# Kernel optimization log

Hardware: AMD Instinct MI355X
Metric: run time of the kernel (lower is better)

The kernel has to match this reference:

```python
import jax, jax.numpy as jnp
import numpy as np

B, N, K = 4, 4096, 16
DP, DM = 128, 512


def _gather(points, idx):
    # points [B,N,C], idx [B,N,K] -> [B,N,K,C] (index_points)
    b, n, k = idx.shape
    flat = jnp.take_along_axis(points, idx.reshape(b, -1)[:, :, None], axis=1)
    return flat.reshape(b, n, k, points.shape[-1])


def _mlp2(x, w1, b1, w2, b2):
    return jax.nn.relu(x @ w1 + b1) @ w2 + b2


def setup_inputs():
    key = jax.random.key(0)
    ks = jax.random.split(key, 20)
    s_dp = 1.0 / np.sqrt(DP)
    s_dm = 1.0 / np.sqrt(DM)
    return {
        "xyz": jax.random.normal(ks[0], (B, N, 3), jnp.float32),
        "features": jax.random.normal(ks[1], (B, N, DP), jnp.float32),
        "fc1_w": jax.random.normal(ks[2], (DP, DM), jnp.float32) * s_dp,
        "fc1_b": jnp.zeros((DM,), jnp.float32),
        "fc2_w": jax.random.normal(ks[3], (DM, DP), jnp.float32) * s_dm,
        "fc2_b": jnp.zeros((DP,), jnp.float32),
        "wq": jax.random.normal(ks[4], (DM, DM), jnp.float32) * s_dm,
        "wk": jax.random.normal(ks[5], (DM, DM), jnp.float32) * s_dm,
        "wv": jax.random.normal(ks[6], (DM, DM), jnp.float32) * s_dm,
        "d1_w": jax.random.normal(ks[7], (3, DM), jnp.float32) * (1.0 / np.sqrt(3.0)),
        "d1_b": jnp.zeros((DM,), jnp.float32),
        "d2_w": jax.random.normal(ks[8], (DM, DM), jnp.float32) * s_dm,
        "d2_b": jnp.zeros((DM,), jnp.float32),
        "g1_w": jax.random.normal(ks[9], (DM, DM), jnp.float32) * s_dm,
        "g1_b": jnp.zeros((DM,), jnp.float32),
        "g2_w": jax.random.normal(ks[10], (DM, DM), jnp.float32) * s_dm,
        "g2_b": jnp.zeros((DM,), jnp.float32),
    }


def reference(xyz, features, fc1_w, fc1_b, fc2_w, fc2_b, wq, wk, wv,
              d1_w, d1_b, d2_w, d2_b, g1_w, g1_b, g2_w, g2_b):
    # square_distance via ||a-b||^2 = |a|^2 + |b|^2 - 2 a.b  (avoids [B,N,N,3])
    sq = jnp.sum(xyz * xyz, axis=-1)                       # [B,N]
    dists = sq[:, :, None] + sq[:, None, :] - 2.0 * jnp.einsum('bnc,bmc->bnm', xyz, xyz)
    knn_idx = jax.lax.top_k(-dists, K)[1]                  # [B,N,K] k-nearest
    knn_xyz = _gather(xyz, knn_idx)                        # [B,N,K,3]

    pre = features
    x = features @ fc1_w + fc1_b                           # [B,N,DM]
    q = x @ wq                                             # [B,N,DM]
    k = _gather(x @ wk, knn_idx)                           # [B,N,K,DM]
    v = _gather(x @ wv, knn_idx)                           # [B,N,K,DM]

    pos_enc = _mlp2(xyz[:, :, None] - knn_xyz, d1_w, d1_b, d2_w, d2_b)  # [B,N,K,DM]
    attn = _mlp2(q[:, :, None] - k + pos_enc, g1_w, g1_b, g2_w, g2_b)   # [B,N,K,DM]
    attn = jax.nn.softmax(attn / np.sqrt(DM), axis=-2)     # softmax over neighbors
    res = jnp.sum(attn * (v + pos_enc), axis=2)            # einsum bmnf,bmnf->bmf
    res = res @ fc2_w + fc2_b + pre                        # [B,N,DP]
    return res, attn
```

## Files before the change

kernel.cpp:

```cpp
#include <hip/hip_runtime.h>

#define NPTS   4096
#define NBATCH 4
#define KNN    16
#define DMODEL 512
#define DPOINT 128
#define QKVLD  1536

#define BN 128
#define BK 64

typedef unsigned short bfu;
typedef __attribute__((ext_vector_type(8))) short short8;
typedef __attribute__((ext_vector_type(4))) float f32x4;

__device__ __forceinline__ bfu f2bf(float f) {
    unsigned u = __builtin_bit_cast(unsigned, f);
    return (bfu)((u + 0x7fffu + ((u >> 16) & 1u)) >> 16);
}
__device__ __forceinline__ float bf2f(bfu h) {
    unsigned u = ((unsigned)h) << 16;
    return __builtin_bit_cast(float, u);
}

__device__ __forceinline__ void gload_lds16(const bfu* g, bfu* l) {
    __builtin_amdgcn_global_load_lds(
        (const __attribute__((address_space(1))) void*)g,
        (__attribute__((address_space(3))) void*)l, 16, 0, 0);
}

#define TPQ 8
#define QPB 32

__device__ __forceinline__ void knn_merge_level(float* bd, int* bi, int lvl)
{
    float pd[KNN]; int pi[KNN];
#pragma unroll
    for (int i = 0; i < KNN; ++i) {
        pd[i] = __shfl_xor(bd[KNN-1-i], lvl);
        pi[i] = __shfl_xor(bi[KNN-1-i], lvl);
    }
#pragma unroll
    for (int i = 0; i < KNN; ++i) {
        bool take = (pd[i] < bd[i]) || (pd[i] == bd[i] && pi[i] < bi[i]);
        if (take) { bd[i] = pd[i]; bi[i] = pi[i]; }
    }
#pragma unroll
    for (int s = 8; s >= 1; s >>= 1) {
#pragma unroll
        for (int i = 0; i < KNN; ++i) {
            if ((i & s) == 0) {
                const int j = i + s;
                bool sw = (bd[j] < bd[i]) || (bd[j] == bd[i] && bi[j] < bi[i]);
                if (sw) {
                    float td = bd[i]; bd[i] = bd[j]; bd[j] = td;
                    int   ti = bi[i]; bi[i] = bi[j]; bi[j] = ti;
                }
            }
        }
    }
}

__global__ __launch_bounds__(256) void knn_kernel(const float* __restrict__ xyz,
                                                  int* __restrict__ knn_out)
{
    __shared__ float4 pts[NPTS];
    const int b    = blockIdx.y;
    const int tid  = threadIdx.x;
    const int qloc = tid >> 3;
    const int sub  = tid & 7;
    const int n    = blockIdx.x * QPB + qloc;

    const float* bx = xyz + (size_t)b * NPTS * 3;
    for (int i = tid; i < NPTS; i += 256) {
        float x = bx[i*3+0], y = bx[i*3+1], z = bx[i*3+2];
        pts[i] = make_float4(x, y, z, x*x + y*y + z*z);
    }
    __syncthreads();

    const float4 me = pts[n];
    float bd[KNN];
    int   bi[KNN];
#pragma unroll
    for (int i = 0; i < KNN; ++i) { bd[i] = 3.4e38f; bi[i] = -1; }

    for (int t0 = 0; t0 < NPTS / TPQ; t0 += 8) {
        float d[8];
#pragma unroll
        for (int j = 0; j < 8; ++j) {
            float4 o = pts[sub + ((t0 + j) << 3)];
            d[j] = me.w + o.w - 2.f*(me.x*o.x + me.y*o.y + me.z*o.z);
        }
        float mn = fminf(fminf(fminf(d[0],d[1]),fminf(d[2],d[3])),
                         fminf(fminf(d[4],d[5]),fminf(d[6],d[7])));
        if (mn < bd[KNN-1]) {
#pragma unroll
            for (int j = 0; j < 8; ++j) {
                float dj = d[j];
                if (dj < bd[KNN-1]) {
                    const int m = sub + ((t0 + j) << 3);
#pragma unroll
                    for (int i = KNN-1; i >= 1; --i) {
                        float dp = bd[i-1];
                        if (dp > dj)        { bd[i] = dp; bi[i] = bi[i-1]; }
                        else if (bd[i] > dj){ bd[i] = dj; bi[i] = m; }
                    }
                    if (bd[0] > dj) { bd[0] = dj; bi[0] = m; }
                }
            }
        }
    }

    knn_merge_level(bd, bi, 1);
    knn_merge_level(bd, bi, 2);
    knn_merge_level(bd, bi, 4);

    int* orow = knn_out + ((size_t)b*NPTS + n) * KNN;
    const int base = b * NPTS;
    orow[sub*2+0] = base + bi[sub*2+0];
    orow[sub*2+1] = base + bi[sub*2+1];
}

__global__ __launch_bounds__(256) void cvt_bf16(const float* __restrict__ src,
                                                bfu* __restrict__ dst, int n4)
{
    int i = blockIdx.x * 256 + threadIdx.x;
    if (i < n4) {
        float4 v = ((const float4*)src)[i];
        bfu* d = dst + (size_t)i * 4;
        d[0] = f2bf(v.x); d[1] = f2bf(v.y); d[2] = f2bf(v.z); d[3] = f2bf(v.w);
    }
}

__global__ __launch_bounds__(256) void transpose_cvt(const float* __restrict__ src,
                                                     bfu* __restrict__ dst,
                                                     int K, int N)
{
    int i = blockIdx.x * 256 + threadIdx.x;
    if (i < K * N) {
        int n = i / K, k = i - n * K;
        dst[i] = f2bf(src[(size_t)k * N + n]);
    }
}

__global__ __launch_bounds__(256) void pos_h_kernel(
    const float* __restrict__ xyz, const int* __restrict__ knng,
    const float* __restrict__ d1w, const float* __restrict__ d1b,
    bfu* __restrict__ out, int row_base)
{
    const int idx  = blockIdx.x * 256 + threadIdx.x;
    const int rloc = idx >> 6;
    const int c0   = (idx & 63) * 8;
    const int grow = row_base + rloc;
    const int p    = grow >> 4;
    const int nb   = knng[grow];
    const float rx = xyz[(size_t)p*3+0] - xyz[(size_t)nb*3+0];
    const float ry = xyz[(size_t)p*3+1] - xyz[(size_t)nb*3+1];
    const float rz = xyz[(size_t)p*3+2] - xyz[(size_t)nb*3+2];
    short8 ov;
#pragma unroll
    for (int j = 0; j < 8; ++j) {
        const int k = c0 + j;
        float v = d1b[k];
        v = fmaf(rx, d1w[k],        v);
        v = fmaf(ry, d1w[512 + k],  v);
        v = fmaf(rz, d1w[1024 + k], v);
        ov[j] = (short)f2bf(fmaxf(v, 0.f));
    }
    *(short8*)&out[(size_t)rloc * DMODEL + c0] = ov;
}

template<int BMt, int ASRC, bool BIAS, bool RELU, bool OUTBF, bool RESID, bool SMAX>
__global__ __launch_bounds__(256) void gemm_mfma(
    const bfu* __restrict__ A, const bfu* __restrict__ BT,
    const float* __restrict__ bias, const float* __restrict__ resid,
    void* __restrict__ Cout, int M, int Kd, int Nd,
    const int* __restrict__ knng,
    const bfu* __restrict__ qb, const bfu* __restrict__ kb,
    const bfu* __restrict__ posc, const bfu* __restrict__ vb,
    bfu* __restrict__ resbuf, int row_base)
{
    constexpr int MF  = BMt / 32;
    constexpr int TPR = 256 / BMt;
    constexpr int RPW = BMt / 4;

    __shared__ bfu As[BMt * BK];
    __shared__ bfu Bs[BN * BK];

    const int tid  = threadIdx.x;
    const int lane = tid & 63;
    const int w    = tid >> 6;

    const int nbn     = Nd / BN;
    const int q8      = gridDim.x >> 3;
    const int logical = (blockIdx.x & 7) * q8 + (blockIdx.x >> 3);
    const int bm      = (logical / nbn) * BMt;
    const int bn      = (logical % nbn) * BN;

    const int wm   = (w >> 1) * (BMt / 2);
    const int wn   = (w & 1) * 64;
    const int lrow = lane & 15;
    const int kgrp = lane >> 4;

    f32x4 acc[MF][4];
#pragma unroll
    for (int m = 0; m < MF; ++m)
#pragma unroll
        for (int n = 0; n < 4; ++n) acc[m][n] = (f32x4){0.f, 0.f, 0.f, 0.f};

    int grow = 0, gnb = 0;
    if constexpr (ASRC == 2) {
        int r = tid / TPR;
        grow  = row_base + bm + r;
        gnb   = knng[grow];
    }

    for (int k0 = 0; k0 < Kd; k0 += BK) {
        __syncthreads();

        {
            int r0 = w * 32;
            const bfu* gB = BT + (size_t)(bn + r0 + (lane >> 3)) * Kd + k0 + (lane & 7) * 8;
            bfu* lB = Bs + r0 * BK;
#pragma unroll
            for (int i = 0; i < 4; ++i)
                gload_lds16(gB + (size_t)i * 8 * Kd, lB + i * 8 * BK);
        }

        if constexpr (ASRC == 0) {
            int r0 = w * RPW;
            const bfu* gA = A + (size_t)(bm + r0 + (lane >> 3)) * Kd + k0 + (lane & 7) * 8;
            bfu* lA = As + r0 * BK;
#pragma unroll
            for (int i = 0; i < RPW / 8; ++i)
                gload_lds16(gA + (size_t)i * 8 * Kd, lA + i * 8 * BK);
        } else {
            constexpr int NC8 = (BK / TPR) / 8;
            int r = tid / TPR, cseg = (tid % TPR) * (BK / TPR);
            int p = grow >> 4;
            const bfu* qrow = qb   + (size_t)p    * QKVLD + k0 + cseg;
            const bfu* krow = kb   + (size_t)gnb  * QKVLD + k0 + cseg;
            const bfu* prow = posc + (size_t)(bm + r) * DMODEL + k0 + cseg;
#pragma unroll
            for (int c8 = 0; c8 < NC8; ++c8) {
                short8 qv = *(const short8*)(qrow + c8 * 8);
                short8 kv = *(const short8*)(krow + c8 * 8);
                short8 pv = *(const short8*)(prow + c8 * 8);
                short8 ov;
#pragma unroll
                for (int j = 0; j < 8; ++j) {
                    float v = bf2f((bfu)qv[j]) - bf2f((bfu)kv[j]) + bf2f((bfu)pv[j]);
                    ov[j] = (short)f2bf(v);
                }
                *(short8*)&As[r * BK + cseg + c8 * 8] = ov;
            }
        }

        __syncthreads();

#pragma unroll
        for (int kk = 0; kk < BK; kk += 32) {
            short8 af[MF], bfr[4];
#pragma unroll
            for (int m = 0; m < MF; ++m)
                af[m] = *(const short8*)&As[(wm + m * 16 + lrow) * BK + kk + kgrp * 8];
#pragma unroll
            for (int n = 0; n < 4; ++n)
                bfr[n] = *(const short8*)&Bs[(wn + n * 16 + lrow) * BK + kk + kgrp * 8];
#pragma unroll
            for (int m = 0; m < MF; ++m)
#pragma unroll
                for (int n = 0; n < 4; ++n)
                    acc[m][n] = __builtin_amdgcn_mfma_f32_16x16x32_bf16(
                        af[m], bfr[n], acc[m][n], 0, 0, 0);
        }
    }

    if constexpr (SMAX) {
        const float scale = 0.044194173824159216f;
#pragma unroll
        for (int m = 0; m < MF; ++m) {
            const int row0 = bm + wm + m * 16 + kgrp * 4;
            const int ploc = (bm + wm + m * 16) >> 4;
            int gnb4[4];
#pragma unroll
            for (int r = 0; r < 4; ++r) gnb4[r] = knng[(size_t)row_base + row0 + r];
#pragma unroll
            for (int n = 0; n < 4; ++n) {
                const int col = bn + wn + n * 16 + lrow;
                const float bv = bias[col];
                float v0 = (acc[m][n][0] + bv) * scale;
                float v1 = (acc[m][n][1] + bv) * scale;
                float v2 = (acc[m][n][2] + bv) * scale;
                float v3 = (acc[m][n][3] + bv) * scale;
                float mx = fmaxf(fmaxf(v0, v1), fmaxf(v2, v3));
                mx = fmaxf(mx, __shfl_xor(mx, 16));
                mx = fmaxf(mx, __shfl_xor(mx, 32));
                float e0 = __expf(v0 - mx), e1 = __expf(v1 - mx);
                float e2 = __expf(v2 - mx), e3 = __expf(v3 - mx);
                float s = e0 + e1 + e2 + e3;
                s += __shfl_xor(s, 16);
                s += __shfl_xor(s, 32);
                const float inv = 1.f / s;
                float a0 = e0*inv, a1 = e1*inv, a2 = e2*inv, a3 = e3*inv;
                float* ao = (float*)Cout;
                ao[(size_t)(row0 + 0) * DMODEL + col] = a0;
                ao[(size_t)(row0 + 1) * DMODEL + col] = a1;
                ao[(size_t)(row0 + 2) * DMODEL + col] = a2;
                ao[(size_t)(row0 + 3) * DMODEL + col] = a3;
                float res = 0.f;
                res = fmaf(a0, bf2f(vb[(size_t)gnb4[0]*QKVLD + col]) + bf2f(posc[(size_t)(row0+0)*DMODEL + col]), res);
                res = fmaf(a1, bf2f(vb[(size_t)gnb4[1]*QKVLD + col]) + bf2f(posc[(size_t)(row0+1)*DMODEL + col]), res);
                res = fmaf(a2, bf2f(vb[(size_t)gnb4[2]*QKVLD + col]) + bf2f(posc[(size_t)(row0+2)*DMODEL + col]), res);
                res = fmaf(a3, bf2f(vb[(size_t)gnb4[3]*QKVLD + col]) + bf2f(posc[(size_t)(row0+3)*DMODEL + col]), res);
                res += __shfl_xor(res, 16);
                res += __shfl_xor(res, 32);
                if (kgrp == 0) {
                    const size_t pglob = (size_t)(row_base >> 4) + ploc;
                    resbuf[pglob * DMODEL + col] = f2bf(res);
                }
            }
        }
        return;
    }

#pragma unroll
    for (int m = 0; m < MF; ++m) {
#pragma unroll
        for (int n = 0; n < 4; ++n) {
            int col = bn + wn + n * 16 + lrow;
            float bv = BIAS ? bias[col] : 0.f;
#pragma unroll
            for (int r = 0; r < 4; ++r) {
                int row = bm + wm + m * 16 + kgrp * 4 + r;
                float v = acc[m][n][r] + bv;
                if (RESID) v += resid[(size_t)row * Nd + col];
                if (RELU)  v = fmaxf(v, 0.f);
                if (OUTBF) ((bfu*)Cout)[(size_t)row * Nd + col] = f2bf(v);
                else     ((float*)Cout)[(size_t)row * Nd + col] = v;
            }
        }
    }
}

extern "C" void kernel_launch(void* const* d_in, const int* in_sizes, int n_in,
                              void* d_out, int out_size, void* d_ws, size_t ws_size,
                              hipStream_t stream)
{
    const float* xyz      = (const float*)d_in[0];
    const float* features = (const float*)d_in[1];
    const float* fc1_w    = (const float*)d_in[2];
    const float* fc1_b    = (const float*)d_in[3];
    const float* fc2_w    = (const float*)d_in[4];
    const float* fc2_b    = (const float*)d_in[5];
    const float* wq       = (const float*)d_in[6];
    const float* wk       = (const float*)d_in[7];
    const float* wv       = (const float*)d_in[8];
    const float* d1_w     = (const float*)d_in[9];
    const float* d1_b     = (const float*)d_in[10];
    const float* d2_w     = (const float*)d_in[11];
    const float* d2_b     = (const float*)d_in[12];
    const float* g1_w     = (const float*)d_in[13];
    const float* g1_b     = (const float*)d_in[14];
    const float* g2_w     = (const float*)d_in[15];
    const float* g2_b     = (const float*)d_in[16];

    const size_t Mpts  = (size_t)NBATCH * NPTS;
    const size_t Mrows = Mpts * KNN;
    float* out_res  = (float*)d_out;
    float* out_attn = (float*)d_out + Mpts * DPOINT;

    size_t off = 0;
    auto ab = [&](size_t elems) { bfu* r = (bfu*)((char*)d_ws + off); off += elems * 2; return r; };
    bfu* fc1T  = ab((size_t)DMODEL * DPOINT);
    bfu* qkvT  = ab((size_t)QKVLD * DMODEL);
    bfu* d2T   = ab((size_t)DMODEL * DMODEL);
    bfu* g1T   = ab((size_t)DMODEL * DMODEL);
    bfu* g2T   = ab((size_t)DMODEL * DMODEL);
    bfu* fc2T  = ab((size_t)DPOINT * DMODEL);
    bfu* featb = ab(Mpts * DPOINT);
    bfu* xb    = ab(Mpts * DMODEL);
    bfu* qkvb  = ab(Mpts * QKVLD);
    bfu* resb  = xb;
    int* knng  = (int*)((char*)d_ws + off); off += Mrows * 4;

    int nchunk = 32;
    {
        const int cands[4] = {4, 8, 16, 32};
        for (int i = 0; i < 4; ++i) {
            size_t need = off + 2ull * (Mrows / cands[i]) * DMODEL * 2;
            if (need <= ws_size) { nchunk = cands[i]; break; }
        }
    }
    const size_t Rc  = Mrows / nchunk;
    bfu* posc = ab(Rc * DMODEL);
    bfu* hc   = ab(Rc * DMODEL);

    knn_kernel<<<dim3(NPTS/QPB, NBATCH), 256, 0, stream>>>(xyz, knng);

    transpose_cvt<<<dim3((DPOINT*DMODEL+255)/256), 256, 0, stream>>>(fc1_w, fc1T, DPOINT, DMODEL);
    transpose_cvt<<<dim3((DMODEL*DMODEL+255)/256), 256, 0, stream>>>(wq, qkvT,                 DMODEL, DMODEL);
    transpose_cvt<<<dim3((DMODEL*DMODEL+255)/256), 256, 0, stream>>>(wk, qkvT +   DMODEL*DMODEL, DMODEL, DMODEL);
    transpose_cvt<<<dim3((DMODEL*DMODEL+255)/256), 256, 0, stream>>>(wv, qkvT + 2*DMODEL*DMODEL, DMODEL, DMODEL);
    transpose_cvt<<<dim3((DMODEL*DMODEL+255)/256), 256, 0, stream>>>(d2_w, d2T, DMODEL, DMODEL);
    transpose_cvt<<<dim3((DMODEL*DMODEL+255)/256), 256, 0, stream>>>(g1_w, g1T, DMODEL, DMODEL);
    transpose_cvt<<<dim3((DMODEL*DMODEL+255)/256), 256, 0, stream>>>(g2_w, g2T, DMODEL, DMODEL);
    transpose_cvt<<<dim3((DMODEL*DPOINT+255)/256), 256, 0, stream>>>(fc2_w, fc2T, DMODEL, DPOINT);
    cvt_bf16<<<dim3((Mpts*DPOINT/4+255)/256), 256, 0, stream>>>(features, featb, (int)(Mpts*DPOINT/4));

#define GARGS(Ap, Bp, biasp, residp, Cp, M_, K_, N_, rb) \
    (Ap), (Bp), (biasp), (residp), (Cp), (int)(M_), (int)(K_), (int)(N_), \
    knng, qkvb, qkvb + DMODEL, posc, qkvb + 2*DMODEL, resb, (int)(rb)

    gemm_mfma<128, 0, true,  false, true,  false, false><<<dim3((Mpts/128)*(DMODEL/BN)), 256, 0, stream>>>(
        GARGS(featb, fc1T, fc1_b, nullptr, xb, Mpts, DPOINT, DMODEL, 0));
    gemm_mfma<128, 0, false, false, true,  false, false><<<dim3((Mpts/128)*(QKVLD/BN)), 256, 0, stream>>>(
        GARGS(xb, qkvT, nullptr, nullptr, qkvb, Mpts, DMODEL, QKVLD, 0));

    for (int c = 0; c < nchunk; ++c) {
        const size_t rb = (size_t)c * Rc;
        float* attn_c = out_attn + rb * DMODEL;

        pos_h_kernel<<<dim3((unsigned)(Rc/4)), 256, 0, stream>>>(xyz, knng, d1_w, d1_b, hc, (int)rb);

#define CHUNK_LAUNCH(BMT) \
        gemm_mfma<BMT, 0, true, false, true, false, false><<<dim3((unsigned)((Rc/BMT)*(DMODEL/BN))), 256, 0, stream>>>( \
            GARGS(hc, d2T, d2_b, nullptr, posc, Rc, DMODEL, DMODEL, rb)); \
        gemm_mfma<BMT, 2, true, true,  true, false, false><<<dim3((unsigned)((Rc/BMT)*(DMODEL/BN))), 256, 0, stream>>>( \
            GARGS(nullptr, g1T, g1_b, nullptr, hc, Rc, DMODEL, DMODEL, rb)); \
        gemm_mfma<BMT, 0, false, false, false, false, true><<<dim3((unsigned)((Rc/BMT)*(DMODEL/BN))), 256, 0, stream>>>( \
            GARGS(hc, g2T, g2_b, nullptr, attn_c, Rc, DMODEL, DMODEL, rb));

        if (Rc >= 32768) { CHUNK_LAUNCH(128) }
        else             { CHUNK_LAUNCH(64)  }
#undef CHUNK_LAUNCH
    }

    gemm_mfma<128, 0, true, false, false, true, false><<<dim3((Mpts/128)*(DPOINT/BN)), 256, 0, stream>>>(
        GARGS(resb, fc2T, fc2_b, features, out_res, Mpts, DMODEL, DPOINT, 0));
#undef GARGS
}
```

Baseline: 1.976 ms.

## Give each kNN query a full wavefront and read precomputed points from global

The kNN kernel now assigns one query per 64-lane wavefront instead of 8 threads per query, so each lane scans 64 candidates and the partial top-16 lists are merged across six shuffle levels. Points with their squared norms are precomputed once by a new pts4 kernel into workspace. The kernel reads them straight from global/L2 instead of staging all 4096 points in LDS per block. This removes the per-block LDS fill and the occupancy limit of 64KB of LDS, and gives much more parallelism. The cost is more cross-lane merge work per query, eight times as many total threads, and uncached global loads in the inner loop.

```diff
diff --git a/kernel.cpp b/kernel.cpp
--- a/kernel.cpp
+++ b/kernel.cpp
@@ -29,8 +29,13 @@
         (__attribute__((address_space(3))) void*)l, 16, 0, 0);
 }
 
-#define TPQ 8
-#define QPB 32
+__global__ __launch_bounds__(256) void pts4_kernel(const float* __restrict__ xyz,
+                                                   float4* __restrict__ pts4)
+{
+    int i = blockIdx.x * 256 + threadIdx.x;
+    float x = xyz[i*3+0], y = xyz[i*3+1], z = xyz[i*3+2];
+    pts4[i] = make_float4(x, y, z, x*x + y*y + z*z);
+}
 
 __device__ __forceinline__ void knn_merge_level(float* bd, int* bi, int lvl)
 {
@@ -61,34 +66,27 @@
     }
 }
 
-__global__ __launch_bounds__(256) void knn_kernel(const float* __restrict__ xyz,
+__global__ __launch_bounds__(256) void knn_kernel(const float4* __restrict__ pts4,
                                                   int* __restrict__ knn_out)
 {
-    __shared__ float4 pts[NPTS];
     const int b    = blockIdx.y;
     const int tid  = threadIdx.x;
-    const int qloc = tid >> 3;
-    const int sub  = tid & 7;
-    const int n    = blockIdx.x * QPB + qloc;
-
-    const float* bx = xyz + (size_t)b * NPTS * 3;
-    for (int i = tid; i < NPTS; i += 256) {
-        float x = bx[i*3+0], y = bx[i*3+1], z = bx[i*3+2];
-        pts[i] = make_float4(x, y, z, x*x + y*y + z*z);
-    }
-    __syncthreads();
-
-    const float4 me = pts[n];
+    const int qloc = tid >> 6;
+    const int lane = tid & 63;
+    const int n    = blockIdx.x * 4 + qloc;
+
+    const float4* bp = pts4 + (size_t)b * NPTS;
+    const float4 me = bp[n];
     float bd[KNN];
     int   bi[KNN];
 #pragma unroll
     for (int i = 0; i < KNN; ++i) { bd[i] = 3.4e38f; bi[i] = -1; }
 
-    for (int t0 = 0; t0 < NPTS / TPQ; t0 += 8) {
+    for (int t0 = 0; t0 < NPTS / 64; t0 += 8) {
         float d[8];
 #pragma unroll
         for (int j = 0; j < 8; ++j) {
-            float4 o = pts[sub + ((t0 + j) << 3)];
+            float4 o = bp[lane + ((t0 + j) << 6)];
             d[j] = me.w + o.w - 2.f*(me.x*o.x + me.y*o.y + me.z*o.z);
         }
         float mn = fminf(fminf(fminf(d[0],d[1]),fminf(d[2],d[3])),
@@ -98,7 +96,7 @@
             for (int j = 0; j < 8; ++j) {
                 float dj = d[j];
                 if (dj < bd[KNN-1]) {
-                    const int m = sub + ((t0 + j) << 3);
+                    const int m = lane + ((t0 + j) << 6);
 #pragma unroll
                     for (int i = KNN-1; i >= 1; --i) {
                         float dp = bd[i-1];
@@ -114,11 +112,15 @@
     knn_merge_level(bd, bi, 1);
     knn_merge_level(bd, bi, 2);
     knn_merge_level(bd, bi, 4);
+    knn_merge_level(bd, bi, 8);
+    knn_merge_level(bd, bi, 16);
+    knn_merge_level(bd, bi, 32);
 
     int* orow = knn_out + ((size_t)b*NPTS + n) * KNN;
-    const int base = b * NPTS;
-    orow[sub*2+0] = base + bi[sub*2+0];
-    orow[sub*2+1] = base + bi[sub*2+1];
+    int v = bi[0];
+#pragma unroll
+    for (int i = 1; i < KNN; ++i) if (lane == i) v = bi[i];
+    if (lane < KNN) orow[lane] = b * NPTS + v;
 }
 
 __global__ __launch_bounds__(256) void cvt_bf16(const float* __restrict__ src,
@@ -372,6 +374,7 @@
 
     size_t off = 0;
     auto ab = [&](size_t elems) { bfu* r = (bfu*)((char*)d_ws + off); off += elems * 2; return r; };
+    float4* pts4 = (float4*)d_ws; off += Mpts * sizeof(float4);
     bfu* fc1T  = ab((size_t)DMODEL * DPOINT);
     bfu* qkvT  = ab((size_t)QKVLD * DMODEL);
     bfu* d2T   = ab((size_t)DMODEL * DMODEL);
@@ -396,7 +399,8 @@
     bfu* posc = ab(Rc * DMODEL);
     bfu* hc   = ab(Rc * DMODEL);
 
-    knn_kernel<<<dim3(NPTS/QPB, NBATCH), 256, 0, stream>>>(xyz, knng);
+    pts4_kernel<<<dim3(Mpts/256), 256, 0, stream>>>(xyz, pts4);
+    knn_kernel<<<dim3(NPTS/4, NBATCH), 256, 0, stream>>>(pts4, knng);
 
     transpose_cvt<<<dim3((DPOINT*DMODEL+255)/256), 256, 0, stream>>>(fc1_w, fc1T, DPOINT, DMODEL);
     transpose_cvt<<<dim3((DMODEL*DMODEL+255)/256), 256, 0, stream>>>(wq, qkvT,                 DMODEL, DMODEL);
```

Result: slower. 2.858 ms (+44.7%).
